# Kernel optimization log

Hardware: AMD Instinct MI355X
Metric: run time of the kernel (lower is better)

Reference implementation:

```python
import jax, jax.numpy as jnp
import numpy as np

N_NODES = 50000
N_EDGES = 800000
D_IN, D_HID, D_OUT = 96, 96, 48


def _gcn_conv(x, src, dst, W, b, num_nodes):
    """PyG GCNConv: h = x @ W; out[dst] += norm * h[src]; out += b.
    Symmetric normalization deg^{-1/2}[src] * deg^{-1/2}[dst], self-loops included
    (src/dst already contain self-loops)."""
    h = x @ W  # [N, d_out]
    deg = jax.ops.segment_sum(jnp.ones_like(dst, dtype=h.dtype), dst,
                              num_segments=num_nodes)  # in-degree incl. self-loop
    dinv = jnp.where(deg > 0, jax.lax.rsqrt(deg), 0.0)
    norm = dinv[src] * dinv[dst]  # [E+N]
    msgs = h[src] * norm[:, None]  # gather + scale (the memory-bound part)
    out = jax.ops.segment_sum(msgs, dst, num_segments=num_nodes)  # scatter-add
    return out + b


def setup_inputs() -> dict:
    key = jax.random.key(0)
    k1, k2, k3, k4 = jax.random.split(key, 4)
    x = jax.random.normal(k1, (N_NODES, D_IN), dtype=jnp.float32)
    edge_index = jax.random.randint(k2, (2, N_EDGES), 0, N_NODES, dtype=jnp.int64)
    # Glorot-ish init for weights, zero bias (matches GCNConv defaults)
    W1 = jax.random.normal(k3, (D_IN, D_HID), dtype=jnp.float32) / np.sqrt(D_IN)
    b1 = jnp.zeros((D_HID,), dtype=jnp.float32)
    W2 = jax.random.normal(k4, (D_HID, D_OUT), dtype=jnp.float32) / np.sqrt(D_HID)
    b2 = jnp.zeros((D_OUT,), dtype=jnp.float32)
    return {"x": x, "edge_index": edge_index, "W1": W1, "b1": b1, "W2": W2, "b2": b2}


def reference(x, edge_index, W1, b1, W2, b2):
    num_nodes = x.shape[0]
    loops = jnp.arange(num_nodes, dtype=edge_index.dtype)
    src = jnp.concatenate([edge_index[0], loops])  # add self-loops
    dst = jnp.concatenate([edge_index[1], loops])
    h = _gcn_conv(x, src, dst, W1, b1, num_nodes)
    h = jax.nn.relu(h)
    # dropout p=0.5 is identity in eval mode (self.training=False)
    out = _gcn_conv(h, src, dst, W2, b2, num_nodes)
    return out
```

## Files before the change

kernel.cpp:

```cpp
#include <hip/hip_runtime.h>
#include <hip/hip_bf16.h>


constexpr int NN = 50000;
constexpr int NE = 800000;
constexpr int DI = 96;
constexpr int DH = 96;
constexpr int DO = 48;

constexpr int BK_SHIFT = 6;
constexpr int NBK      = (NN + 63) >> 6;
constexpr int BK_CAP   = 2048;

constexpr int NCHUNK = 256;
constexpr int CH     = (NE + NCHUNK - 1) / NCHUNK;

constexpr int G1_ROWS = 64;
constexpr int NG1     = (NN + G1_ROWS - 1) / G1_ROWS;

typedef unsigned short us4 __attribute__((ext_vector_type(4)));
typedef unsigned short us8 __attribute__((ext_vector_type(8)));

__device__ __forceinline__ float bf2f(unsigned short u) {
    return __uint_as_float(((unsigned int)u) << 16);
}
__device__ __forceinline__ unsigned short f2bf(float f) {
    __hip_bfloat16 b = __float2bfloat16(f);
    return *reinterpret_cast<unsigned short*>(&b);
}


__global__ __launch_bounds__(256) void k_hist(const int* __restrict__ dst,
                                              int* __restrict__ C, int e) {
    __shared__ int hist[NBK];
    for (int i = threadIdx.x; i < NBK; i += 256) hist[i] = 0;
    __syncthreads();
    const int blk = blockIdx.x;
    const int beg = blk * CH, end = min(beg + CH, e);
    for (int i = beg + threadIdx.x; i < end; i += 256)
        atomicAdd(&hist[dst[i] >> BK_SHIFT], 1);
    __syncthreads();
    for (int b = threadIdx.x; b < NBK; b += 256)
        C[b * NCHUNK + blk] = hist[b];
}

__global__ __launch_bounds__(256) void k_rowscan(int* __restrict__ C,
                                                 int* __restrict__ totals,
                                                 int* __restrict__ row_ptr) {
    if (blockIdx.x == 0 && threadIdx.x == 0) row_ptr[NN] = NE;
    const int w    = threadIdx.x >> 6;
    const int lane = threadIdx.x & 63;
    const int r    = blockIdx.x * 4 + w;
    if (r >= NBK) return;
    int* row = C + r * NCHUNK;
    int v[4], s[4];
#pragma unroll
    for (int q = 0; q < 4; ++q) { v[q] = row[q * 64 + lane]; s[q] = v[q]; }
#pragma unroll
    for (int off = 1; off < 64; off <<= 1) {
#pragma unroll
        for (int q = 0; q < 4; ++q) {
            int y = __shfl_up(s[q], off);
            if (lane >= off) s[q] += y;
        }
    }
    int c0 = __shfl(s[0], 63);
    int c1 = __shfl(s[1], 63);
    int c2 = __shfl(s[2], 63);
    s[1] += c0;
    s[2] += c0 + c1;
    s[3] += c0 + c1 + c2;
#pragma unroll
    for (int q = 0; q < 4; ++q) row[q * 64 + lane] = s[q] - v[q];
    if (lane == 63) totals[r] = s[3];
}

__global__ __launch_bounds__(256) void k_scatter_gemm1(
        const int* __restrict__ src, const int* __restrict__ dst,
        const int* __restrict__ C, const int* __restrict__ totals,
        int* __restrict__ bk_ptr, unsigned* __restrict__ ebuf, int e,
        const float* __restrict__ X, const float* __restrict__ W,
        unsigned short* __restrict__ H, int n) {
    __shared__ int bkL[NBK + 1];
    __shared__ int part[256];
    __shared__ int cur[NBK];
    constexpr int P = 97;
    __shared__ float ws[DI * DH];
    __shared__ float xs[G1_ROWS * P];

    const int t = threadIdx.x;

    if (blockIdx.x < NCHUNK) {
        int v[4];
        int s = 0;
        const int base = t * 4;
#pragma unroll
        for (int i = 0; i < 4; ++i) {
            int idx = base + i;
            v[i] = (idx < NBK) ? totals[idx] : 0;
            s += v[i];
        }
        part[t] = s;
        __syncthreads();
#pragma unroll
        for (int off = 1; off < 256; off <<= 1) {
            int x = part[t];
            int a = (t >= off) ? part[t - off] : 0;
            __syncthreads();
            part[t] = x + a;
            __syncthreads();
        }
        int run = part[t] - s;
#pragma unroll
        for (int i = 0; i < 4; ++i) {
            int idx = base + i;
            if (idx <= NBK) bkL[idx] = run;
            run += v[i];
        }
        __syncthreads();

        const int blk = blockIdx.x;
        for (int b = t; b < NBK; b += 256) cur[b] = bkL[b] + C[b * NCHUNK + blk];
        if (blk == 0)
            for (int i = t; i <= NBK; i += 256) bk_ptr[i] = bkL[i];
        __syncthreads();

        const int beg = blk * CH, end = min(beg + CH, e);
        for (int i = beg + t; i < end; i += 256) {
            int d = dst[i];
            int b = d >> BK_SHIFT;
            int pos = atomicAdd(&cur[b], 1);
            ebuf[pos] = ((unsigned)(d & 63) << 16) | (unsigned)src[i];
        }
    } else {
        const int row0 = (blockIdx.x - NCHUNK) * G1_ROWS;
        unsigned short* hout = reinterpret_cast<unsigned short*>(xs);

        for (int i = t; i < DI * DH; i += 256) ws[i] = W[i];
        {
            const float4* Xv = reinterpret_cast<const float4*>(X + (size_t)row0 * DI);
            const int nv   = G1_ROWS * DI / 4;
            const int maxv = ((n - row0) * DI) / 4;
            for (int i = t; i < nv; i += 256) {
                float4 v = (i < maxv) ? Xv[i] : float4{0.f, 0.f, 0.f, 0.f};
                int r = i / 24, c = (i % 24) * 4;
                xs[r * P + c + 0] = v.x;
                xs[r * P + c + 1] = v.y;
                xs[r * P + c + 2] = v.z;
                xs[r * P + c + 3] = v.w;
            }
        }
        __syncthreads();

        const int cg = t & 15, rg = t >> 4;
        float acc[4][6] = {};
#pragma unroll 2
        for (int k = 0; k < DI; ++k) {
            float xv[4];
#pragma unroll
            for (int i = 0; i < 4; ++i) xv[i] = xs[(rg * 4 + i) * P + k];
#pragma unroll
            for (int j = 0; j < 6; ++j) {
                float wv = ws[k * DH + cg * 6 + j];
#pragma unroll
                for (int i = 0; i < 4; ++i) acc[i][j] += xv[i] * wv;
            }
        }
        __syncthreads();

#pragma unroll
        for (int i = 0; i < 4; ++i) {
#pragma unroll
            for (int j = 0; j < 6; ++j)
                hout[(rg * 4 + i) * 96 + cg * 6 + j] = f2bf(acc[i][j]);
        }
        __syncthreads();

        {
            const us8* ho8 = reinterpret_cast<const us8*>(hout);
            us8* H8 = reinterpret_cast<us8*>(H + (size_t)row0 * DH);
            const int nv   = G1_ROWS * DH / 8;
            const int maxv = ((n - row0) * DH) / 8;
            for (int i = t; i < nv && i < maxv; i += 256) H8[i] = ho8[i];
        }
    }
}

__global__ __launch_bounds__(256) void k_bsort(const unsigned* __restrict__ ebuf,
                                               const int* __restrict__ bk_ptr,
                                               int* __restrict__ row_ptr,
                                               float* __restrict__ dinv,
                                               unsigned short* __restrict__ src16, int n) {
    __shared__ unsigned eL[BK_CAP];
    __shared__ unsigned short outL[BK_CAP];
    __shared__ int curL[64];
    __shared__ int baseL[64];

    const int b   = blockIdx.x;
    const int beg = bk_ptr[b];
    const int m   = bk_ptr[b + 1] - beg;
    const int t   = threadIdx.x;

    if (t < 64) curL[t] = 0;
    __syncthreads();

    for (int i = t; i < m; i += 256) {
        unsigned v = ebuf[beg + i];
        eL[i] = v;
        atomicAdd(&curL[v >> 16], 1);
    }
    __syncthreads();

    if (t < 64) {
        int c = curL[t];
        int x = c;
#pragma unroll
        for (int off = 1; off < 64; off <<= 1) {
            int y = __shfl_up(x, off);
            if (t >= off) x += y;
        }
        int excl = x - c;
        baseL[t] = excl;
        int d0 = (b << BK_SHIFT) + t;
        if (d0 < n) {
            row_ptr[d0] = beg + excl;
            dinv[d0]    = rsqrtf((float)(c + 1));
        }
    }
    __syncthreads();
    if (t < 64) curL[t] = baseL[t];
    __syncthreads();

    for (int i = t; i < m; i += 256) {
        unsigned v = eL[i];
        int p = atomicAdd(&curL[v >> 16], 1);
        outL[p] = (unsigned short)(v & 0xFFFFu);
    }
    __syncthreads();
    for (int i = t; i < m; i += 256) src16[beg + i] = outL[i];
}

__global__ __launch_bounds__(256) void k_pack(const unsigned short* __restrict__ src16,
                                              const float* __restrict__ dinv,
                                              unsigned* __restrict__ epack, int e) {
    int i2 = (blockIdx.x * 256 + threadIdx.x) * 2;
    if (i2 + 1 < e) {
        unsigned pairv = *reinterpret_cast<const unsigned*>(src16 + i2);
        unsigned s0 = pairv & 0xFFFFu;
        unsigned s1 = pairv >> 16;
        unsigned w0 = f2bf(dinv[s0]);
        unsigned w1 = f2bf(dinv[s1]);
        uint2 o;
        o.x = (w0 << 16) | s0;
        o.y = (w1 << 16) | s1;
        *reinterpret_cast<uint2*>(epack + i2) = o;
    } else if (i2 < e) {
        unsigned s0 = src16[i2];
        epack[i2] = ((unsigned)f2bf(dinv[s0]) << 16) | s0;
    }
}


__global__ __launch_bounds__(256) void k_agg1(const unsigned short* __restrict__ h1,
                                              const float* __restrict__ dinv,
                                              const int* __restrict__ row_ptr,
                                              const unsigned* __restrict__ epack,
                                              const float* __restrict__ b1,
                                              unsigned short* __restrict__ a1, int n) {
    constexpr int G = 12;
    int t = blockIdx.x * blockDim.x + threadIdx.x;
    if (t >= n * G) return;
    const int node = t / G;
    const int g    = t % G;

    const us8* h8 = reinterpret_cast<const us8*>(h1);
    const float di = dinv[node];

    float accA[8], accB[8];
    {
        us8 hv = h8[(size_t)node * G + g];
#pragma unroll
        for (int j = 0; j < 8; ++j) { accA[j] = di * bf2f(hv[j]); accB[j] = 0.f; }
    }

    const int beg = row_ptr[node];
    const int end = row_ptr[node + 1];
    int k = beg;
    int kA = min((beg + 7) & ~7, end);
    for (; k < kA; ++k) {
        unsigned ev = epack[k];
        float w = bf2f((unsigned short)(ev >> 16));
        us8 vv = h8[(size_t)(ev & 0xFFFFu) * G + g];
#pragma unroll
        for (int j = 0; j < 8; ++j) accA[j] += w * bf2f(vv[j]);
    }
    for (; k + 8 <= end; k += 8) {
        const uint4* ev4 = reinterpret_cast<const uint4*>(epack + k);
        uint4 e0 = ev4[0], e1 = ev4[1];
        us8 v0 = h8[(size_t)(e0.x & 0xFFFFu) * G + g];
        us8 v1 = h8[(size_t)(e0.y & 0xFFFFu) * G + g];
        us8 v2 = h8[(size_t)(e0.z & 0xFFFFu) * G + g];
        us8 v3 = h8[(size_t)(e0.w & 0xFFFFu) * G + g];
        us8 v4 = h8[(size_t)(e1.x & 0xFFFFu) * G + g];
        us8 v5 = h8[(size_t)(e1.y & 0xFFFFu) * G + g];
        us8 v6 = h8[(size_t)(e1.z & 0xFFFFu) * G + g];
        us8 v7 = h8[(size_t)(e1.w & 0xFFFFu) * G + g];
        float w0 = bf2f((unsigned short)(e0.x >> 16));
        float w1 = bf2f((unsigned short)(e0.y >> 16));
        float w2 = bf2f((unsigned short)(e0.z >> 16));
        float w3 = bf2f((unsigned short)(e0.w >> 16));
        float w4 = bf2f((unsigned short)(e1.x >> 16));
        float w5 = bf2f((unsigned short)(e1.y >> 16));
        float w6 = bf2f((unsigned short)(e1.z >> 16));
        float w7 = bf2f((unsigned short)(e1.w >> 16));
#pragma unroll
        for (int j = 0; j < 8; ++j) {
            accA[j] += w0 * bf2f(v0[j]) + w1 * bf2f(v1[j])
                     + w4 * bf2f(v4[j]) + w5 * bf2f(v5[j]);
            accB[j] += w2 * bf2f(v2[j]) + w3 * bf2f(v3[j])
                     + w6 * bf2f(v6[j]) + w7 * bf2f(v7[j]);
        }
    }
    for (; k < end; ++k) {
        unsigned ev = epack[k];
        float w = bf2f((unsigned short)(ev >> 16));
        us8 vv = h8[(size_t)(ev & 0xFFFFu) * G + g];
#pragma unroll
        for (int j = 0; j < 8; ++j) accB[j] += w * bf2f(vv[j]);
    }

    us8 o;
#pragma unroll
    for (int j = 0; j < 8; ++j) {
        float r = di * (accA[j] + accB[j]) + b1[g * 8 + j];
        o[j] = f2bf(fmaxf(r, 0.f));
    }
    reinterpret_cast<us8*>(a1)[(size_t)node * G + g] = o;
}


__global__ __launch_bounds__(256) void k_gemm2(const unsigned short* __restrict__ A,
                                               const float* __restrict__ W,
                                               const float* __restrict__ dinv,
                                               unsigned short* __restrict__ H, int n) {
    constexpr int ROWS = 64, P = 98;
    __shared__ float ws[DH * DO];
    __shared__ unsigned short xs[ROWS * P];

    const int tid  = threadIdx.x;
    const int row0 = blockIdx.x * ROWS;

    for (int i = tid; i < DH * DO; i += 256) ws[i] = W[i];
    {
        const us8* Av = reinterpret_cast<const us8*>(A + (size_t)row0 * DH);
        const int nv   = ROWS * DH / 8;
        const int maxv = ((n - row0) * DH) / 8;
        for (int i = tid; i < nv; i += 256) {
            us8 v = (i < maxv) ? Av[i] : (us8)(0);
            int r = i / 12, c = (i % 12) * 8;
#pragma unroll
            for (int jj = 0; jj < 8; ++jj) xs[r * P + c + jj] = v[jj];
        }
    }
    __syncthreads();

    const int cg = tid & 15, rg = tid >> 4;
    float acc[4][3] = {};
#pragma unroll 2
    for (int k = 0; k < DH; ++k) {
        float xv[4];
#pragma unroll
        for (int i = 0; i < 4; ++i) xv[i] = bf2f(xs[(rg * 4 + i) * P + k]);
#pragma unroll
        for (int j = 0; j < 3; ++j) {
            float wv = ws[k * DO + cg * 3 + j];
#pragma unroll
            for (int i = 0; i < 4; ++i) acc[i][j] += xv[i] * wv;
        }
    }
    __syncthreads();

    unsigned short* hout = xs;
#pragma unroll
    for (int i = 0; i < 4; ++i) {
        int row = row0 + rg * 4 + i;
        float dv = (row < n) ? dinv[row] : 0.f;
#pragma unroll
        for (int j = 0; j < 3; ++j)
            hout[(rg * 4 + i) * 48 + cg * 3 + j] = f2bf(acc[i][j] * dv);
    }
    __syncthreads();

    {
        const us8* ho8 = reinterpret_cast<const us8*>(hout);
        us8* H8 = reinterpret_cast<us8*>(H + (size_t)row0 * DO);
        const int nv   = ROWS * DO / 8;
        const int maxv = ((n - row0) * DO) / 8;
        for (int i = tid; i < nv && i < maxv; i += 256) H8[i] = ho8[i];
    }
}


__global__ __launch_bounds__(256) void k_agg2(const unsigned short* __restrict__ h,
                                              const float* __restrict__ dinv,
                                              const int* __restrict__ row_ptr,
                                              const unsigned short* __restrict__ src16,
                                              const float* __restrict__ bias,
                                              float* __restrict__ outp, int n) {
    constexpr int G = 6;
    int t = blockIdx.x * blockDim.x + threadIdx.x;
    if (t >= n * G) return;
    const int node = t / G;
    const int g    = t % G;

    const us8* h8 = reinterpret_cast<const us8*>(h);

    float accA[8], accB[8];
    {
        us8 hv = h8[(size_t)node * G + g];
#pragma unroll
        for (int j = 0; j < 8; ++j) { accA[j] = bf2f(hv[j]); accB[j] = 0.f; }
    }

    const int beg = row_ptr[node];
    const int end = row_ptr[node + 1];
    int k = beg;
    int kA = min((beg + 7) & ~7, end);
    for (; k < kA; ++k) {
        us8 vv = h8[(size_t)src16[k] * G + g];
#pragma unroll
        for (int j = 0; j < 8; ++j) accA[j] += bf2f(vv[j]);
    }
    for (; k + 8 <= end; k += 8) {
        us8 si = *reinterpret_cast<const us8*>(src16 + k);
        us8 v0 = h8[(size_t)si[0] * G + g];
        us8 v1 = h8[(size_t)si[1] * G + g];
        us8 v2 = h8[(size_t)si[2] * G + g];
        us8 v3 = h8[(size_t)si[3] * G + g];
        us8 v4 = h8[(size_t)si[4] * G + g];
        us8 v5 = h8[(size_t)si[5] * G + g];
        us8 v6 = h8[(size_t)si[6] * G + g];
        us8 v7 = h8[(size_t)si[7] * G + g];
#pragma unroll
        for (int j = 0; j < 8; ++j) {
            accA[j] += (bf2f(v0[j]) + bf2f(v1[j])) + (bf2f(v4[j]) + bf2f(v5[j]));
            accB[j] += (bf2f(v2[j]) + bf2f(v3[j])) + (bf2f(v6[j]) + bf2f(v7[j]));
        }
    }
    for (; k < end; ++k) {
        us8 vv = h8[(size_t)src16[k] * G + g];
#pragma unroll
        for (int j = 0; j < 8; ++j) accB[j] += bf2f(vv[j]);
    }

    const float di = dinv[node];
    const float4* b4 = reinterpret_cast<const float4*>(bias);
    float4 b0 = b4[g * 2], b1 = b4[g * 2 + 1];
    float r[8];
#pragma unroll
    for (int j = 0; j < 8; ++j) r[j] = di * (accA[j] + accB[j]);
    r[0] += b0.x; r[1] += b0.y; r[2] += b0.z; r[3] += b0.w;
    r[4] += b1.x; r[5] += b1.y; r[6] += b1.z; r[7] += b1.w;
    float4* o4 = reinterpret_cast<float4*>(outp + (size_t)node * DO + g * 8);
    o4[0] = float4{r[0], r[1], r[2], r[3]};
    o4[1] = float4{r[4], r[5], r[6], r[7]};
}


extern "C" void kernel_launch(void* const* d_in, const int* in_sizes, int n_in,
                              void* d_out, int out_size, void* d_ws, size_t ws_size,
                              hipStream_t stream) {
    const float* x   = (const float*)d_in[0];
    const int*   ei  = (const int*)d_in[1];
    const float* W1  = (const float*)d_in[2];
    const float* b1  = (const float*)d_in[3];
    const float* W2  = (const float*)d_in[4];
    const float* b2  = (const float*)d_in[5];
    float*       out = (float*)d_out;

    const int* srcv = ei;
    const int* dstv = ei + NE;

    char* p = (char*)d_ws;
    float*          dinv  = (float*)p;           p += (size_t)NN * 4;
    unsigned short* h1    = (unsigned short*)p;  p += (size_t)NN * DH * 2;
    unsigned short* a1    = (unsigned short*)p;  p += (size_t)NN * DH * 2;
    unsigned short* h2    = (unsigned short*)p;  p += (size_t)NN * DO * 2;
    int*      row_ptr     = (int*)p;             p += (size_t)(NN + 16) * 4;
    unsigned short* src16 = (unsigned short*)p;  p += (size_t)NE * 2;
    unsigned* epack       = (unsigned*)p;        p += (size_t)NE * 4;
    unsigned* ebuf        = (unsigned*)p;        p += (size_t)NE * 4;
    int*      Cm          = (int*)p;             p += (size_t)NBK * NCHUNK * 4;
    int*      totals      = (int*)p;             p += (size_t)NBK * 4;
    int*      bk_ptr      = (int*)p;             p += (size_t)(NBK + 1) * 4;

    const int B = 256;

    k_hist<<<NCHUNK, B, 0, stream>>>(dstv, Cm, NE);
    k_rowscan<<<(NBK + 3) / 4, B, 0, stream>>>(Cm, totals, row_ptr);
    k_scatter_gemm1<<<NCHUNK + NG1, B, 0, stream>>>(
        srcv, dstv, Cm, totals, bk_ptr, ebuf, NE, x, W1, h1, NN);
    k_bsort<<<NBK, B, 0, stream>>>(ebuf, bk_ptr, row_ptr, dinv, src16, NN);
    k_pack<<<(NE / 2 + B - 1) / B, B, 0, stream>>>(src16, dinv, epack, NE);

    {
        int total = NN * 12;
        k_agg1<<<(total + B - 1) / B, B, 0, stream>>>(
            h1, dinv, row_ptr, epack, b1, a1, NN);
    }
    k_gemm2<<<(NN + 63) / 64, B, 0, stream>>>(a1, W2, dinv, h2, NN);
    {
        int total = NN * 6;
        k_agg2<<<(total + B - 1) / B, B, 0, stream>>>(
            h2, dinv, row_ptr, src16, b2, out, NN);
    }
}
```

Measured before the change: 125.3 us.

## Split layer-1 aggregation into three feature-slice passes and shrink GEMM1 tiles

```diff
diff --git a/kernel.cpp b/kernel.cpp
--- a/kernel.cpp
+++ b/kernel.cpp
@@ -15,7 +15,7 @@
 constexpr int NCHUNK = 256;
 constexpr int CH     = (NE + NCHUNK - 1) / NCHUNK;
 
-constexpr int G1_ROWS = 64;
+constexpr int G1_ROWS = 32;
 constexpr int NG1     = (NN + G1_ROWS - 1) / G1_ROWS;
 
 typedef unsigned short us4 __attribute__((ext_vector_type(4)));
@@ -81,16 +81,16 @@
         int* __restrict__ bk_ptr, unsigned* __restrict__ ebuf, int e,
         const float* __restrict__ X, const float* __restrict__ W,
         unsigned short* __restrict__ H, int n) {
-    __shared__ int bkL[NBK + 1];
-    __shared__ int part[256];
-    __shared__ int cur[NBK];
     constexpr int P = 97;
-    __shared__ float ws[DI * DH];
-    __shared__ float xs[G1_ROWS * P];
+    __shared__ __align__(16) char smem[(DI * DH + G1_ROWS * P) * 4];
 
     const int t = threadIdx.x;
 
     if (blockIdx.x < NCHUNK) {
+        int* bkL  = reinterpret_cast<int*>(smem);
+        int* part = bkL + (NBK + 1);
+        int* cur  = part + 256;
+
         int v[4];
         int s = 0;
         const int base = t * 4;
@@ -133,8 +133,11 @@
             ebuf[pos] = ((unsigned)(d & 63) << 16) | (unsigned)src[i];
         }
     } else {
+        float* ws = reinterpret_cast<float*>(smem);
+        float* xs = ws + DI * DH;
+        unsigned short* hout = reinterpret_cast<unsigned short*>(xs);
+
         const int row0 = (blockIdx.x - NCHUNK) * G1_ROWS;
-        unsigned short* hout = reinterpret_cast<unsigned short*>(xs);
 
         for (int i = t; i < DI * DH; i += 256) ws[i] = W[i];
         {
@@ -153,26 +156,26 @@
         __syncthreads();
 
         const int cg = t & 15, rg = t >> 4;
-        float acc[4][6] = {};
+        float acc[2][6] = {};
 #pragma unroll 2
         for (int k = 0; k < DI; ++k) {
-            float xv[4];
-#pragma unroll
-            for (int i = 0; i < 4; ++i) xv[i] = xs[(rg * 4 + i) * P + k];
+            float xv[2];
+#pragma unroll
+            for (int i = 0; i < 2; ++i) xv[i] = xs[(rg * 2 + i) * P + k];
 #pragma unroll
             for (int j = 0; j < 6; ++j) {
                 float wv = ws[k * DH + cg * 6 + j];
 #pragma unroll
-                for (int i = 0; i < 4; ++i) acc[i][j] += xv[i] * wv;
+                for (int i = 0; i < 2; ++i) acc[i][j] += xv[i] * wv;
             }
         }
         __syncthreads();
 
 #pragma unroll
-        for (int i = 0; i < 4; ++i) {
+        for (int i = 0; i < 2; ++i) {
 #pragma unroll
             for (int j = 0; j < 6; ++j)
-                hout[(rg * 4 + i) * 96 + cg * 6 + j] = f2bf(acc[i][j]);
+                hout[(rg * 2 + i) * 96 + cg * 6 + j] = f2bf(acc[i][j]);
         }
         __syncthreads();
 
@@ -261,24 +264,25 @@
 }
 
 
-__global__ __launch_bounds__(256) void k_agg1(const unsigned short* __restrict__ h1,
-                                              const float* __restrict__ dinv,
-                                              const int* __restrict__ row_ptr,
-                                              const unsigned* __restrict__ epack,
-                                              const float* __restrict__ b1,
-                                              unsigned short* __restrict__ a1, int n) {
-    constexpr int G = 12;
-    int t = blockIdx.x * blockDim.x + threadIdx.x;
-    if (t >= n * G) return;
-    const int node = t / G;
-    const int g    = t % G;
+__global__ __launch_bounds__(256) void k_agg1_pass(
+        const unsigned short* __restrict__ h1,
+        const float* __restrict__ dinv,
+        const int* __restrict__ row_ptr,
+        const unsigned* __restrict__ epack,
+        const float* __restrict__ b1,
+        unsigned short* __restrict__ a1, int n, int pass) {
+    int t = blockIdx.x * 256 + threadIdx.x;
+    if (t >= n * 4) return;
+    const int node = t >> 2;
+    const int g    = t & 3;
+    const int off  = pass * 4 + g;
 
     const us8* h8 = reinterpret_cast<const us8*>(h1);
     const float di = dinv[node];
 
     float accA[8], accB[8];
     {
-        us8 hv = h8[(size_t)node * G + g];
+        us8 hv = h8[(size_t)node * 12 + off];
 #pragma unroll
         for (int j = 0; j < 8; ++j) { accA[j] = di * bf2f(hv[j]); accB[j] = 0.f; }
     }
@@ -290,21 +294,21 @@
     for (; k < kA; ++k) {
         unsigned ev = epack[k];
         float w = bf2f((unsigned short)(ev >> 16));
-        us8 vv = h8[(size_t)(ev & 0xFFFFu) * G + g];
+        us8 vv = h8[(size_t)(ev & 0xFFFFu) * 12 + off];
 #pragma unroll
         for (int j = 0; j < 8; ++j) accA[j] += w * bf2f(vv[j]);
     }
     for (; k + 8 <= end; k += 8) {
         const uint4* ev4 = reinterpret_cast<const uint4*>(epack + k);
         uint4 e0 = ev4[0], e1 = ev4[1];
-        us8 v0 = h8[(size_t)(e0.x & 0xFFFFu) * G + g];
-        us8 v1 = h8[(size_t)(e0.y & 0xFFFFu) * G + g];
-        us8 v2 = h8[(size_t)(e0.z & 0xFFFFu) * G + g];
-        us8 v3 = h8[(size_t)(e0.w & 0xFFFFu) * G + g];
-        us8 v4 = h8[(size_t)(e1.x & 0xFFFFu) * G + g];
-        us8 v5 = h8[(size_t)(e1.y & 0xFFFFu) * G + g];
-        us8 v6 = h8[(size_t)(e1.z & 0xFFFFu) * G + g];
-        us8 v7 = h8[(size_t)(e1.w & 0xFFFFu) * G + g];
+        us8 v0 = h8[(size_t)(e0.x & 0xFFFFu) * 12 + off];
+        us8 v1 = h8[(size_t)(e0.y & 0xFFFFu) * 12 + off];
+        us8 v2 = h8[(size_t)(e0.z & 0xFFFFu) * 12 + off];
+        us8 v3 = h8[(size_t)(e0.w & 0xFFFFu) * 12 + off];
+        us8 v4 = h8[(size_t)(e1.x & 0xFFFFu) * 12 + off];
+        us8 v5 = h8[(size_t)(e1.y & 0xFFFFu) * 12 + off];
+        us8 v6 = h8[(size_t)(e1.z & 0xFFFFu) * 12 + off];
+        us8 v7 = h8[(size_t)(e1.w & 0xFFFFu) * 12 + off];
         float w0 = bf2f((unsigned short)(e0.x >> 16));
         float w1 = bf2f((unsigned short)(e0.y >> 16));
         float w2 = bf2f((unsigned short)(e0.z >> 16));
@@ -324,7 +328,7 @@
     for (; k < end; ++k) {
         unsigned ev = epack[k];
         float w = bf2f((unsigned short)(ev >> 16));
-        us8 vv = h8[(size_t)(ev & 0xFFFFu) * G + g];
+        us8 vv = h8[(size_t)(ev & 0xFFFFu) * 12 + off];
 #pragma unroll
         for (int j = 0; j < 8; ++j) accB[j] += w * bf2f(vv[j]);
     }
@@ -332,10 +336,10 @@
     us8 o;
 #pragma unroll
     for (int j = 0; j < 8; ++j) {
-        float r = di * (accA[j] + accB[j]) + b1[g * 8 + j];
+        float r = di * (accA[j] + accB[j]) + b1[pass * 32 + g * 8 + j];
         o[j] = f2bf(fmaxf(r, 0.f));
     }
-    reinterpret_cast<us8*>(a1)[(size_t)node * G + g] = o;
+    reinterpret_cast<us8*>(a1)[(size_t)node * 12 + off] = o;
 }
 
 
@@ -504,11 +508,14 @@
     k_pack<<<(NE / 2 + B - 1) / B, B, 0, stream>>>(src16, dinv, epack, NE);
 
     {
-        int total = NN * 12;
-        k_agg1<<<(total + B - 1) / B, B, 0, stream>>>(
-            h1, dinv, row_ptr, epack, b1, a1, NN);
-    }
+        const int NBA = (NN * 4 + B - 1) / B;
+        for (int pass = 0; pass < 3; ++pass)
+            k_agg1_pass<<<NBA, B, 0, stream>>>(
+                h1, dinv, row_ptr, epack, b1, a1, NN, pass);
+    }
+
     k_gemm2<<<(NN + 63) / 64, B, 0, stream>>>(a1, W2, dinv, h2, NN);
+
     {
         int total = NN * 6;
         k_agg2<<<(total + B - 1) / B, B, 0, stream>>>(
```

New measurement: 143.9 us. 14.9% more time.
